# Kernel optimization log

Hardware: AMD Instinct MI355X
Metric: run time of the kernel (lower is better)

## Reference

```python
import jax, jax.numpy as jnp
import numpy as np

HIDDEN = 5120
HEAD_DIM = 128
HQ = 40
HKV = 8
NUM_MOD = 3
Q_SIZE = HQ * HEAD_DIM          # 5120
KV_SIZE = HKV * HEAD_DIM        # 1024
GATE = HQ                       # attn gating enabled
QKV_OUT = Q_SIZE + 2 * KV_SIZE + GATE  # 7208
EPS = 1e-6
N_TOK = 2048


def setup_inputs() -> dict:
    key = jax.random.key(0)
    ks = jax.random.split(key, 8)
    s = 0.02
    return {
        "hidden_states": jax.random.normal(ks[0], (N_TOK, HIDDEN), jnp.float32),
        "rope": jax.random.normal(ks[1], (N_TOK, HEAD_DIM), jnp.float32),
        "pre_norm_w": jax.random.normal(ks[2], (NUM_MOD * HIDDEN,), jnp.float32) * s,
        "qkv_w": jax.random.normal(ks[3], (NUM_MOD * QKV_OUT, HIDDEN), jnp.float32) * s,
        "q_norm_w": jax.random.normal(ks[4], (NUM_MOD * HEAD_DIM,), jnp.float32) * s,
        "k_norm_w": jax.random.normal(ks[5], (NUM_MOD * HEAD_DIM,), jnp.float32) * s,
        "proj_w": jax.random.normal(ks[6], (NUM_MOD * HIDDEN, Q_SIZE), jnp.float32) * s,
        "modality_ids": jax.random.randint(ks[7], (N_TOK,), 0, NUM_MOD, jnp.int64),
    }


def _mm_rmsnorm(x, w_flat, mids, dim):
    # per-token modality weight slice; residual parameterization (w + 1)
    w = w_flat.reshape(NUM_MOD, dim)[mids]  # [N, dim]
    if x.ndim == 3:
        w = w[:, None, :]  # broadcast over heads
    rms = jax.lax.rsqrt(jnp.mean(x * x, axis=-1, keepdims=True) + EPS)
    return x * rms * (w + 1.0)


def _moe_linear(x, w_flat, mids, out_f):
    # 3 GEMMs (one per expert), then per-token select -- same math as masked dispatch
    wm = w_flat.reshape(NUM_MOD, out_f, x.shape[-1])
    outs = jnp.einsum('nd,mod->nmo', x, wm)  # [N, 3, out_f]
    return jnp.take_along_axis(outs, mids[:, None, None], axis=1)[:, 0, :]


def _rotary(x, cos, sin):
    # x: [N, H, D]; cos/sin: [N, D/2]
    x1, x2 = jnp.split(x, 2, axis=-1)
    c = cos[:, None, :]
    s = sin[:, None, :]
    return jnp.concatenate([x1 * c - x2 * s, x1 * s + x2 * c], axis=-1)


def reference(hidden_states, rope, pre_norm_w, qkv_w, q_norm_w, k_norm_w, proj_w, modality_ids):
    N = hidden_states.shape[0]
    mids = modality_ids

    h = _mm_rmsnorm(hidden_states, pre_norm_w, mids, HIDDEN)
    qkv = _moe_linear(h, qkv_w, mids, QKV_OUT)  # [N, 7208]
    q, k, v, g = jnp.split(qkv, [Q_SIZE, Q_SIZE + KV_SIZE, Q_SIZE + 2 * KV_SIZE], axis=-1)
    q = q.reshape(N, HQ, HEAD_DIM)
    k = k.reshape(N, HKV, HEAD_DIM)
    v = v.reshape(N, HKV, HEAD_DIM)

    q = _mm_rmsnorm(q, q_norm_w, mids, HEAD_DIM)
    k = _mm_rmsnorm(k, k_norm_w, mids, HEAD_DIM)

    sin, cos = jnp.split(rope, 2, axis=-1)  # rope.chunk(2, dim=-1) -> sin, cos
    q = _rotary(q, cos, sin)
    k = _rotary(k, cos, sin)

    # GQA attention over the full token sequence
    G = HQ // HKV
    qg = q.reshape(N, HKV, G, HEAD_DIM)
    scale = 1.0 / np.sqrt(HEAD_DIM).astype(np.float32)
    scores = jnp.einsum('nkgd,mkd->kgnm', qg, k) * scale  # [8, 5, N, N]
    p = jax.nn.softmax(scores, axis=-1)
    o = jnp.einsum('kgnm,mkd->nkgd', p, v).reshape(N, HQ, HEAD_DIM)

    o = o * jax.nn.sigmoid(g)[:, :, None]  # attention gating per q-head
    o = o.reshape(N, Q_SIZE)
    return _moe_linear(o, proj_w, mids, HIDDEN)
```

## Files before the change

kernel.cpp:

```cpp
#include <hip/hip_runtime.h>
#include <hip/hip_bf16.h>

#define N_TOK 2048
#define HIDDEN 5120
#define HEAD_DIM 128
#define HQ 40
#define HKV 8
#define QKV_OUT 7208
#define Q_SIZE 5120
#define KV_SIZE 1024

typedef __attribute__((ext_vector_type(8))) short bf16x8;
typedef __attribute__((ext_vector_type(4))) float f32x4;
typedef __attribute__((ext_vector_type(4))) unsigned short us4;

__device__ inline unsigned short f2bf(float f) {
    return __builtin_bit_cast(unsigned short, __float2bfloat16(f));
}
__device__ inline float bf2f(unsigned short s) {
    unsigned u = ((unsigned)s) << 16;
    return __builtin_bit_cast(float, u);
}
__device__ inline f32x4 mfma16(bf16x8 a, bf16x8 b, f32x4 c) {
    return __builtin_amdgcn_mfma_f32_16x16x32_bf16(a, b, c, 0, 0, 0);
}
__device__ inline void gl16(const void* g, void* l) {
    __builtin_amdgcn_global_load_lds((__attribute__((address_space(1))) void*)g,
                                     (__attribute__((address_space(3))) void*)l, 16, 0, 0);
}

__global__ void k_sort(const int* __restrict__ mids_raw, int* __restrict__ meta,
                       int* __restrict__ perm) {
    int l = threadIdx.x;
    int oddnz = 0;
    for (int c = 0; c < 32; ++c) {
        int idx = c * 64 + l;
        int v = mids_raw[idx];
        if ((idx & 1) && v != 0) oddnz = 1;
    }
    bool is64 = (__ballot(oddnz) == 0ULL);
    int c0 = 0, c1 = 0;
    for (int c = 0; c < 32; ++c) {
        int i = c * 64 + l;
        int m = is64 ? mids_raw[2 * i] : mids_raw[i];
        c0 += (m == 0); c1 += (m == 1);
    }
    for (int o = 32; o; o >>= 1) { c0 += __shfl_xor(c0, o); c1 += __shfl_xor(c1, o); }
    if (l == 0) { meta[0] = 0; meta[1] = c0; meta[2] = c0 + c1; meta[3] = N_TOK; }
    int r0 = 0, r1 = c0, r2 = c0 + c1;
    unsigned long long below = (1ULL << l) - 1ULL;
    for (int c = 0; c < 32; ++c) {
        int i = c * 64 + l;
        int m = is64 ? mids_raw[2 * i] : mids_raw[i];
        unsigned long long b0 = __ballot(m == 0), b1 = __ballot(m == 1), b2 = __ballot(m == 2);
        int pos = (m == 0) ? r0 + __popcll(b0 & below)
                : (m == 1) ? r1 + __popcll(b1 & below)
                           : r2 + __popcll(b2 & below);
        perm[pos] = i;
        r0 += __popcll(b0); r1 += __popcll(b1); r2 += __popcll(b2);
    }
}

__global__ __launch_bounds__(256) void k_cvt(const float* __restrict__ src,
                                             unsigned short* __restrict__ dst, int n8) {
    int i = blockIdx.x * 256 + threadIdx.x;
    int stride = gridDim.x * 256;
    for (; i < n8; i += stride) {
        float4 a = ((const float4*)src)[2 * i];
        float4 b = ((const float4*)src)[2 * i + 1];
        bf16x8 o;
        o[0] = (short)f2bf(a.x); o[1] = (short)f2bf(a.y);
        o[2] = (short)f2bf(a.z); o[3] = (short)f2bf(a.w);
        o[4] = (short)f2bf(b.x); o[5] = (short)f2bf(b.y);
        o[6] = (short)f2bf(b.z); o[7] = (short)f2bf(b.w);
        ((bf16x8*)dst)[i] = o;
    }
}

__global__ __launch_bounds__(256) void k_prenorm(const float* __restrict__ hidden,
        const float* __restrict__ pnw, const int* __restrict__ meta,
        const int* __restrict__ perm, unsigned short* __restrict__ h) {
    int i = blockIdx.x;
    int m = (i >= meta[1]) + (i >= meta[2]);
    int t = perm[i];
    const float4* x = (const float4*)(hidden + (size_t)t * HIDDEN);
    const float4* wv = (const float4*)(pnw + (size_t)m * HIDDEN);
    int tid = threadIdx.x;
    float4 xv[5];
    float ss = 0.f;
#pragma unroll
    for (int j = 0; j < 5; ++j) {
        xv[j] = x[tid + j * 256];
        ss += xv[j].x * xv[j].x + xv[j].y * xv[j].y + xv[j].z * xv[j].z + xv[j].w * xv[j].w;
    }
    for (int o = 32; o; o >>= 1) ss += __shfl_xor(ss, o);
    __shared__ float red[4];
    if ((tid & 63) == 0) red[tid >> 6] = ss;
    __syncthreads();
    float rms = rsqrtf((red[0] + red[1] + red[2] + red[3]) * (1.f / HIDDEN) + 1e-6f);
    us4* dst = (us4*)(h + (size_t)i * HIDDEN);
#pragma unroll
    for (int j = 0; j < 5; ++j) {
        float4 w = wv[tid + j * 256];
        us4 o4;
        o4.x = f2bf(xv[j].x * rms * (w.x + 1.f));
        o4.y = f2bf(xv[j].y * rms * (w.y + 1.f));
        o4.z = f2bf(xv[j].z * rms * (w.z + 1.f));
        o4.w = f2bf(xv[j].w * rms * (w.w + 1.f));
        dst[tid + j * 256] = o4;
    }
}

template <int NOUT, bool SCATTER>
__global__ __launch_bounds__(256, 2) void k_gemm(
        const unsigned short* __restrict__ A, const unsigned short* __restrict__ Bw,
        unsigned short* __restrict__ outB, float* __restrict__ outF,
        const int* __restrict__ meta, const int* __restrict__ perm,
        int nx, int ny) {
    int nwg = nx * ny * 3;
    int bid = blockIdx.x;
    int xcd = bid & 7, o = bid >> 3;
    int q = nwg >> 3, r = nwg & 7;
    int swz = (xcd < r ? xcd * (q + 1) : r * (q + 1) + (xcd - r) * q) + o;
    int mz = swz / (nx * ny);
    int rest = swz - mz * (nx * ny);
    int ty = rest / nx, tx = rest - ty * nx;

    int rowS = meta[mz], rowE = meta[mz + 1];
    int row0 = rowS + tx * 128;
    if (row0 >= rowE) return;
    int col0 = ty * 128;
    const unsigned short* Bm = Bw + (size_t)mz * NOUT * HIDDEN;

    __shared__ __align__(16) char smem[65536];
    int tid = threadIdx.x, l = tid & 63, w = tid >> 6;
    int wr = (w >> 1) * 64, wc = (w & 1) * 64;

    f32x4 acc[4][4] = {};

    const int lr = l >> 3, lc = l & 7;
    const int sch = (lc ^ lr) * 8;
    const unsigned short* ag[4];
    const unsigned short* bg[4];
#pragma unroll
    for (int j = 0; j < 4; ++j) {
        int ar = row0 + 32 * j + 8 * w + lr;
        if (ar > rowE - 1) ar = rowE - 1;
        ag[j] = A + (size_t)ar * HIDDEN + sch;
        int bc = col0 + 32 * j + 8 * w + lr;
        if (bc > NOUT - 1) bc = NOUT - 1;
        bg[j] = Bm + (size_t)bc * HIDDEN + sch;
    }
    char* asw = smem + w * 1024;
    char* bsw = smem + 16384 + w * 1024;

    auto STAGE = [&](int buf, int kk) {
#pragma unroll
        for (int j = 0; j < 4; ++j) {
            gl16(ag[j] + kk, asw + buf * 32768 + j * 4096);
            gl16(bg[j] + kk, bsw + buf * 32768 + j * 4096);
        }
    };
    auto COMPUTE = [&](int buf) {
        char* baseA = smem + buf * 32768;
        char* baseB = baseA + 16384;
#pragma unroll
        for (int ks = 0; ks < 2; ++ks) {
            bf16x8 af[4], bfm[4];
#pragma unroll
            for (int mi = 0; mi < 4; ++mi) {
                int row = wr + mi * 16 + (l & 15);
                af[mi] = *(const bf16x8*)(baseA + row * 128 +
                            ((ks * 64 + (l >> 4) * 16) ^ ((row & 7) << 4)));
            }
#pragma unroll
            for (int ni = 0; ni < 4; ++ni) {
                int row = wc + ni * 16 + (l & 15);
                bfm[ni] = *(const bf16x8*)(baseB + row * 128 +
                            ((ks * 64 + (l >> 4) * 16) ^ ((row & 7) << 4)));
            }
#pragma unroll
            for (int mi = 0; mi < 4; ++mi)
#pragma unroll
                for (int ni = 0; ni < 4; ++ni)
                    acc[mi][ni] = mfma16(af[mi], bfm[ni], acc[mi][ni]);
        }
    };

    STAGE(0, 0);
    asm volatile("s_waitcnt vmcnt(0)" ::: "memory");
    __builtin_amdgcn_sched_barrier(0);
    __builtin_amdgcn_s_barrier();
    __builtin_amdgcn_sched_barrier(0);
    int cur = 0;
#pragma unroll 1
    for (int kt = 0; kt < HIDDEN / 64 - 1; ++kt) {
        STAGE(cur ^ 1, (kt + 1) * 64);
        COMPUTE(cur);
        asm volatile("s_waitcnt vmcnt(0) lgkmcnt(0)" ::: "memory");
        __builtin_amdgcn_sched_barrier(0);
        __builtin_amdgcn_s_barrier();
        __builtin_amdgcn_sched_barrier(0);
        cur ^= 1;
    }
    COMPUTE(cur);

#pragma unroll
    for (int mi = 0; mi < 4; ++mi) {
        int rbase = row0 + wr + mi * 16 + ((l >> 4) << 2);
#pragma unroll
        for (int ni = 0; ni < 4; ++ni) {
            int col = col0 + wc + ni * 16 + (l & 15);
            if (col >= NOUT) continue;
#pragma unroll
            for (int rr = 0; rr < 4; ++rr) {
                int row = rbase + rr;
                if (row >= rowE) continue;
                if (SCATTER) {
                    int t = perm[row];
                    outF[(size_t)t * HIDDEN + col] = acc[mi][ni][rr];
                } else {
                    outB[(size_t)row * NOUT + col] = f2bf(acc[mi][ni][rr]);
                }
            }
        }
    }
}

template <int NOUT, bool SCATTER>
__global__ __launch_bounds__(256) void k_moe_gemm(
        const unsigned short* __restrict__ A, const float* __restrict__ B,
        unsigned short* __restrict__ outB, float* __restrict__ outF,
        const int* __restrict__ meta, const int* __restrict__ perm) {
    int mz = blockIdx.z;
    int rowS = meta[mz], rowE = meta[mz + 1];
    int row0 = rowS + blockIdx.y * 128;
    if (row0 >= rowE) return;
    int col0 = blockIdx.x * 128;
    const float* Bm = B + (size_t)mz * NOUT * HIDDEN;

    __shared__ __align__(16) unsigned short As[128 * 64];
    __shared__ __align__(16) unsigned short Bs[128 * 64];
    int tid = threadIdx.x, l = tid & 63, w = tid >> 6;
    int wr = (w >> 1) * 64, wc = (w & 1) * 64;

    f32x4 acc[4][4] = {};
    int sr = tid >> 1, half = tid & 1;
    int arow = row0 + sr;
    if (arow > N_TOK - 1) arow = N_TOK - 1;
    const unsigned short* aptr = A + (size_t)arow * HIDDEN + half * 32;
    int bcol = col0 + sr;
    bool bok = (bcol < NOUT);
    const float* bptr = Bm + (size_t)(bok ? bcol : 0) * HIDDEN + half * 32;

    char* awp[4]; char* bwp[4];
#pragma unroll
    for (int q = 0; q < 4; ++q) {
        int boff = sr * 128 + ((((half * 4 + q) * 16)) ^ ((sr & 7) << 4));
        awp[q] = (char*)As + boff;
        bwp[q] = (char*)Bs + boff;
    }

#pragma unroll 1
    for (int kk = 0; kk < HIDDEN; kk += 64) {
        bf16x8 av[4];
#pragma unroll
        for (int q = 0; q < 4; ++q) av[q] = *(const bf16x8*)(aptr + kk + q * 8);
        bf16x8 bw[4];
#pragma unroll
        for (int q = 0; q < 4; ++q) {
            float4 u, v;
            if (bok) {
                u = ((const float4*)(bptr + kk))[2 * q];
                v = ((const float4*)(bptr + kk))[2 * q + 1];
            } else {
                u = make_float4(0.f, 0.f, 0.f, 0.f);
                v = u;
            }
            bf16x8 pk;
            pk[0] = (short)f2bf(u.x); pk[1] = (short)f2bf(u.y);
            pk[2] = (short)f2bf(u.z); pk[3] = (short)f2bf(u.w);
            pk[4] = (short)f2bf(v.x); pk[5] = (short)f2bf(v.y);
            pk[6] = (short)f2bf(v.z); pk[7] = (short)f2bf(v.w);
            bw[q] = pk;
        }
        __syncthreads();
#pragma unroll
        for (int q = 0; q < 4; ++q) {
            *(bf16x8*)awp[q] = av[q];
            *(bf16x8*)bwp[q] = bw[q];
        }
        __syncthreads();
#pragma unroll
        for (int ks = 0; ks < 2; ++ks) {
            bf16x8 af[4], bfm[4];
#pragma unroll
            for (int mi = 0; mi < 4; ++mi) {
                int row = wr + mi * 16 + (l & 15);
                af[mi] = *(const bf16x8*)((char*)As + row * 128 +
                            ((ks * 64 + (l >> 4) * 16) ^ ((row & 7) << 4)));
            }
#pragma unroll
            for (int ni = 0; ni < 4; ++ni) {
                int row = wc + ni * 16 + (l & 15);
                bfm[ni] = *(const bf16x8*)((char*)Bs + row * 128 +
                            ((ks * 64 + (l >> 4) * 16) ^ ((row & 7) << 4)));
            }
#pragma unroll
            for (int mi = 0; mi < 4; ++mi)
#pragma unroll
                for (int ni = 0; ni < 4; ++ni)
                    acc[mi][ni] = mfma16(af[mi], bfm[ni], acc[mi][ni]);
        }
    }
#pragma unroll
    for (int mi = 0; mi < 4; ++mi) {
        int rbase = row0 + wr + mi * 16 + ((l >> 4) << 2);
#pragma unroll
        for (int ni = 0; ni < 4; ++ni) {
            int col = col0 + wc + ni * 16 + (l & 15);
            if (col >= NOUT) continue;
#pragma unroll
            for (int rr = 0; rr < 4; ++rr) {
                int row = rbase + rr;
                if (row >= rowE) continue;
                if (SCATTER) {
                    int t = perm[row];
                    outF[(size_t)t * HIDDEN + col] = acc[mi][ni][rr];
                } else {
                    outB[(size_t)row * NOUT + col] = f2bf(acc[mi][ni][rr]);
                }
            }
        }
    }
}

__global__ __launch_bounds__(256) void k_qknorm(const unsigned short* __restrict__ qkv,
        const float* __restrict__ rope, const float* __restrict__ qnw,
        const float* __restrict__ knw, const int* __restrict__ meta,
        const int* __restrict__ perm, unsigned short* __restrict__ qb,
        unsigned short* __restrict__ kb, float* __restrict__ gate) {
    int i = blockIdx.x;
    int m = (i >= meta[1]) + (i >= meta[2]);
    int t = perm[i];
    int tid = threadIdx.x, w = tid >> 6, l = tid & 63;
    const unsigned short* base = qkv + (size_t)i * QKV_OUT;
    const float* rp = rope + (size_t)t * HEAD_DIM;
    const float qscale = 0.08838834764831845f * 1.4426950408889634f;
    for (int hh = w; hh < 48; hh += 4) {
        bool isq = hh < 40;
        const unsigned short* src = base + (isq ? hh * 128 : Q_SIZE + (hh - 40) * 128);
        float x0 = bf2f(src[2 * l]), x1 = bf2f(src[2 * l + 1]);
        float ss = x0 * x0 + x1 * x1;
        for (int o = 32; o; o >>= 1) ss += __shfl_xor(ss, o);
        float rms = rsqrtf(ss * (1.f / 128.f) + 1e-6f);
        const float* nw = (isq ? qnw : knw) + m * 128;
        float y0 = x0 * rms * (nw[2 * l] + 1.f);
        float y1 = x1 * rms * (nw[2 * l + 1] + 1.f);
        float p0 = __shfl_xor(y0, 32);
        float p1 = __shfl_xor(y1, 32);
        float r0v, r1v;
        if (l < 32) {
            int d = 2 * l;
            r0v = y0 * rp[64 + d] - p0 * rp[d];
            r1v = y1 * rp[64 + d + 1] - p1 * rp[d + 1];
        } else {
            int d = 2 * l - 64;
            r0v = p0 * rp[d] + y0 * rp[64 + d];
            r1v = p1 * rp[d + 1] + y1 * rp[64 + d + 1];
        }
        if (isq) {
            r0v *= qscale; r1v *= qscale;
            unsigned short* dst = qb + (size_t)i * Q_SIZE + hh * 128 + 2 * l;
            dst[0] = f2bf(r0v); dst[1] = f2bf(r1v);
        } else {
            unsigned short* dst = kb + (size_t)i * KV_SIZE + (hh - 40) * 128 + 2 * l;
            dst[0] = f2bf(r0v); dst[1] = f2bf(r1v);
        }
    }
    if (tid < HQ) {
        float g = bf2f(base[Q_SIZE + 2 * KV_SIZE + tid]);
        gate[(size_t)i * HQ + tid] = 1.f / (1.f + expf(-g));
    }
}

__global__ __launch_bounds__(256) void k_vtrans(const unsigned short* __restrict__ qkv,
                                                unsigned short* __restrict__ vT) {
    int t0 = blockIdx.x * 64, db = blockIdx.y * 64, kvh = blockIdx.z;
    __shared__ unsigned short tile[64][68];
    int tid = threadIdx.x;
    int tr = tid >> 2, seg = tid & 3;
    const unsigned short* src = qkv + (size_t)(t0 + tr) * QKV_OUT + Q_SIZE + KV_SIZE +
                                kvh * 128 + db + seg * 16;
    us4* drow = (us4*)&tile[tr][seg * 16];
#pragma unroll
    for (int q = 0; q < 4; ++q) drow[q] = ((const us4*)src)[q];
    __syncthreads();
    int dr = tid >> 2;
    unsigned short* dst = vT + ((size_t)kvh * 128 + db + dr) * N_TOK + t0 + seg * 16;
    unsigned short buf[16];
#pragma unroll
    for (int j = 0; j < 16; ++j) buf[j] = tile[seg * 16 + j][dr];
#pragma unroll
    for (int q = 0; q < 4; ++q) ((us4*)dst)[q] = ((us4*)buf)[q];
}

__global__ __launch_bounds__(256) void k_attn(
        const unsigned short* __restrict__ qb,
        const unsigned short* __restrict__ kb,
        const unsigned short* __restrict__ vT,
        const float* __restrict__ gate,
        unsigned short* __restrict__ og) {
    int qt = blockIdx.x, qh = blockIdx.y, kvh = qh / 5;
    int tid = threadIdx.x, w = tid >> 6, l = tid & 63;
    int q0 = qt * 128 + w * 32;
    __shared__ __align__(16) char smem[49152];
    char* Ks = smem;
    char* Vs = smem + 16384;
    char* Ps = smem + 32768 + w * 4096;

    bf16x8 qf[2][4];
#pragma unroll
    for (int mi = 0; mi < 2; ++mi)
#pragma unroll
        for (int ks = 0; ks < 4; ++ks)
            qf[mi][ks] = *(const bf16x8*)(qb + (size_t)(q0 + mi * 16 + (l & 15)) * Q_SIZE +
                                          qh * 128 + ks * 32 + (l >> 4) * 8);

    f32x4 oacc[2][8] = {};
    f32x4 psum[2] = {};

    int kr = tid >> 2, kseg = tid & 3;
    int vr = tid >> 1, vh2 = tid & 1;

#pragma unroll 1
    for (int kt = 0; kt < 32; ++kt) {
        int t0 = kt * 64;
        bf16x8 kv4[4], vv4[4];
        const unsigned short* ksrc = kb + (size_t)(t0 + kr) * KV_SIZE + kvh * 128 + kseg * 32;
        const unsigned short* vsrc = vT + ((size_t)kvh * 128 + vr) * N_TOK + t0 + vh2 * 32;
#pragma unroll
        for (int q = 0; q < 4; ++q) {
            kv4[q] = *(const bf16x8*)(ksrc + q * 8);
            vv4[q] = *(const bf16x8*)(vsrc + q * 8);
        }
        __syncthreads();
#pragma unroll
        for (int q = 0; q < 4; ++q) {
            *(bf16x8*)(Ks + kr * 256 + ((((kseg * 4 + q) * 16)) ^ ((kr & 7) << 4))) = kv4[q];
            *(bf16x8*)(Vs + vr * 128 + ((((vh2 * 4 + q) * 16)) ^ ((vr & 7) << 4))) = vv4[q];
        }
        __syncthreads();
        f32x4 s[2][4] = {};
#pragma unroll
        for (int ks = 0; ks < 4; ++ks) {
            bf16x8 kf[4];
#pragma unroll
            for (int ni = 0; ni < 4; ++ni) {
                int row = ni * 16 + (l & 15);
                kf[ni] = *(const bf16x8*)(Ks + row * 256 +
                            ((ks * 64 + (l >> 4) * 16) ^ ((row & 7) << 4)));
            }
#pragma unroll
            for (int mi = 0; mi < 2; ++mi)
#pragma unroll
                for (int ni = 0; ni < 4; ++ni)
                    s[mi][ni] = mfma16(qf[mi][ks], kf[ni], s[mi][ni]);
        }
#pragma unroll
        for (int mi = 0; mi < 2; ++mi)
#pragma unroll
            for (int ni = 0; ni < 4; ++ni) {
#pragma unroll
                for (int r = 0; r < 4; ++r) {
                    float p = exp2f(s[mi][ni][r]);
                    psum[mi][r] += p;
                    int qr = mi * 16 + ((l >> 4) << 2) + r;
                    int tcb = (ni * 16 + (l & 15)) * 2;
                    *(unsigned short*)(Ps + qr * 128 +
                        (tcb ^ (((qr >> 2) & 3) << 5))) = f2bf(p);
                }
            }
#pragma unroll
        for (int ks = 0; ks < 2; ++ks) {
            bf16x8 pa[2];
#pragma unroll
            for (int mi = 0; mi < 2; ++mi) {
                int qr = mi * 16 + (l & 15);
                pa[mi] = *(const bf16x8*)(Ps + qr * 128 +
                            ((ks * 64 + (l >> 4) * 16) ^ (((qr >> 2) & 3) << 5)));
            }
#pragma unroll
            for (int nd = 0; nd < 8; ++nd) {
                int row = nd * 16 + (l & 15);
                bf16x8 vf = *(const bf16x8*)(Vs + row * 128 +
                            ((ks * 64 + (l >> 4) * 16) ^ ((row & 7) << 4)));
#pragma unroll
                for (int mi = 0; mi < 2; ++mi)
                    oacc[mi][nd] = mfma16(pa[mi], vf, oacc[mi][nd]);
            }
        }
    }
#pragma unroll
    for (int mi = 0; mi < 2; ++mi)
#pragma unroll
        for (int r = 0; r < 4; ++r) {
            float v = psum[mi][r];
            v += __shfl_xor(v, 1);
            v += __shfl_xor(v, 2);
            v += __shfl_xor(v, 4);
            v += __shfl_xor(v, 8);
            psum[mi][r] = v;
        }
#pragma unroll
    for (int mi = 0; mi < 2; ++mi)
#pragma unroll
        for (int r = 0; r < 4; ++r) {
            int row = q0 + mi * 16 + ((l >> 4) << 2) + r;
            float sc = (1.f / psum[mi][r]) * gate[(size_t)row * HQ + qh];
#pragma unroll
            for (int nd = 0; nd < 8; ++nd)
                og[(size_t)row * Q_SIZE + qh * 128 + nd * 16 + (l & 15)] =
                    f2bf(oacc[mi][nd][r] * sc);
        }
}

extern "C" void kernel_launch(void* const* d_in, const int* in_sizes, int n_in,
                              void* d_out, int out_size, void* d_ws, size_t ws_size,
                              hipStream_t stream) {
    const float* hidden = (const float*)d_in[0];
    const float* rope   = (const float*)d_in[1];
    const float* pnw    = (const float*)d_in[2];
    const float* qkvw   = (const float*)d_in[3];
    const float* qnw    = (const float*)d_in[4];
    const float* knw    = (const float*)d_in[5];
    const float* projw  = (const float*)d_in[6];
    const int*   mids   = (const int*)d_in[7];
    float* out = (float*)d_out;

    char* ws = (char*)d_ws;
    const size_t nqkvw = (size_t)3 * QKV_OUT * HIDDEN;
    const size_t nprojw = (size_t)3 * HIDDEN * Q_SIZE;
    const size_t wbytes = (nqkvw + nprojw) * 2;

    const size_t small_bytes = 16384 +
        (size_t)N_TOK * HIDDEN * 2 +
        (size_t)N_TOK * QKV_OUT * 2 +
        (size_t)N_TOK * Q_SIZE * 2 +
        (size_t)N_TOK * KV_SIZE * 2 +
        (size_t)N_TOK * KV_SIZE * 2 +
        (size_t)N_TOK * Q_SIZE * 2 +
        (size_t)N_TOK * HQ * 4;
    bool use_bf = (ws_size >= wbytes + small_bytes);
    if (!use_bf && ws_size < small_bytes) return;

    unsigned short* wqkv = (unsigned short*)ws;
    unsigned short* wproj = wqkv + nqkvw;
    char* sb = ws + (use_bf ? wbytes : 0);

    int* meta = (int*)sb;
    int* perm = (int*)(sb + 64);
    unsigned short* h   = (unsigned short*)(sb + 16384);
    unsigned short* qkv = h   + (size_t)N_TOK * HIDDEN;
    unsigned short* qb  = qkv + (size_t)N_TOK * QKV_OUT;
    unsigned short* kb  = qb  + (size_t)N_TOK * Q_SIZE;
    unsigned short* vT  = kb  + (size_t)N_TOK * KV_SIZE;
    unsigned short* og  = vT  + (size_t)N_TOK * KV_SIZE;
    float* gate = (float*)(og + (size_t)N_TOK * Q_SIZE);

    k_sort<<<1, 64, 0, stream>>>(mids, meta, perm);
    if (use_bf) {
        k_cvt<<<2048, 256, 0, stream>>>(qkvw, wqkv, (int)(nqkvw / 8));
        k_cvt<<<2048, 256, 0, stream>>>(projw, wproj, (int)(nprojw / 8));
    }
    k_prenorm<<<2048, 256, 0, stream>>>(hidden, pnw, meta, perm, h);
    if (use_bf)
        k_gemm<QKV_OUT, false><<<16 * 57 * 3, 256, 0, stream>>>(
            h, wqkv, qkv, nullptr, meta, perm, 16, 57);
    else
        k_moe_gemm<QKV_OUT, false><<<dim3(57, 16, 3), 256, 0, stream>>>(
            h, qkvw, qkv, nullptr, meta, perm);
    k_qknorm<<<2048, 256, 0, stream>>>(qkv, rope, qnw, knw, meta, perm, qb, kb, gate);
    k_vtrans<<<dim3(32, 2, 8), 256, 0, stream>>>(qkv, vT);
    k_attn<<<dim3(16, 40), 256, 0, stream>>>(qb, kb, vT, gate, og);
    if (use_bf)
        k_gemm<HIDDEN, true><<<16 * 40 * 3, 256, 0, stream>>>(
            og, wproj, nullptr, out, meta, perm, 16, 40);
    else
        k_moe_gemm<HIDDEN, true><<<dim3(40, 16, 3), 256, 0, stream>>>(
            og, projw, nullptr, out, meta, perm);
}
```

Before: 958.6 us.

## Fuse fp32-to-bf16 weight conversion into the MoE GEMM B-tile load

```diff
diff --git a/kernel.cpp b/kernel.cpp
--- a/kernel.cpp
+++ b/kernel.cpp
@@ -61,22 +61,6 @@
     }
 }
 
-__global__ __launch_bounds__(256) void k_cvt(const float* __restrict__ src,
-                                             unsigned short* __restrict__ dst, int n8) {
-    int i = blockIdx.x * 256 + threadIdx.x;
-    int stride = gridDim.x * 256;
-    for (; i < n8; i += stride) {
-        float4 a = ((const float4*)src)[2 * i];
-        float4 b = ((const float4*)src)[2 * i + 1];
-        bf16x8 o;
-        o[0] = (short)f2bf(a.x); o[1] = (short)f2bf(a.y);
-        o[2] = (short)f2bf(a.z); o[3] = (short)f2bf(a.w);
-        o[4] = (short)f2bf(b.x); o[5] = (short)f2bf(b.y);
-        o[6] = (short)f2bf(b.z); o[7] = (short)f2bf(b.w);
-        ((bf16x8*)dst)[i] = o;
-    }
-}
-
 __global__ __launch_bounds__(256) void k_prenorm(const float* __restrict__ hidden,
         const float* __restrict__ pnw, const int* __restrict__ meta,
         const int* __restrict__ perm, unsigned short* __restrict__ h) {
@@ -113,7 +97,7 @@
 
 template <int NOUT, bool SCATTER>
 __global__ __launch_bounds__(256, 2) void k_gemm(
-        const unsigned short* __restrict__ A, const unsigned short* __restrict__ Bw,
+        const unsigned short* __restrict__ A, const float* __restrict__ Bw,
         unsigned short* __restrict__ outB, float* __restrict__ outF,
         const int* __restrict__ meta, const int* __restrict__ perm,
         int nx, int ny) {
@@ -130,7 +114,7 @@
     int row0 = rowS + tx * 128;
     if (row0 >= rowE) return;
     int col0 = ty * 128;
-    const unsigned short* Bm = Bw + (size_t)mz * NOUT * HIDDEN;
+    const float* Bm = Bw + (size_t)mz * NOUT * HIDDEN;
 
     __shared__ __align__(16) char smem[65536];
     int tid = threadIdx.x, l = tid & 63, w = tid >> 6;
@@ -141,24 +125,44 @@
     const int lr = l >> 3, lc = l & 7;
     const int sch = (lc ^ lr) * 8;
     const unsigned short* ag[4];
-    const unsigned short* bg[4];
 #pragma unroll
     for (int j = 0; j < 4; ++j) {
         int ar = row0 + 32 * j + 8 * w + lr;
         if (ar > rowE - 1) ar = rowE - 1;
         ag[j] = A + (size_t)ar * HIDDEN + sch;
+    }
+    const float* bg[4];
+    int brow[4];
+#pragma unroll
+    for (int j = 0; j < 4; ++j) {
         int bc = col0 + 32 * j + 8 * w + lr;
         if (bc > NOUT - 1) bc = NOUT - 1;
-        bg[j] = Bm + (size_t)bc * HIDDEN + sch;
+        bg[j] = Bm + (size_t)bc * HIDDEN + lc * 8;
+        brow[j] = 32 * j + 8 * w + lr;
     }
     char* asw = smem + w * 1024;
-    char* bsw = smem + 16384 + w * 1024;
-
+
+    float4 breg[4][2];
     auto STAGE = [&](int buf, int kk) {
 #pragma unroll
+        for (int j = 0; j < 4; ++j) gl16(ag[j] + kk, asw + buf * 32768 + j * 4096);
+#pragma unroll
         for (int j = 0; j < 4; ++j) {
-            gl16(ag[j] + kk, asw + buf * 32768 + j * 4096);
-            gl16(bg[j] + kk, bsw + buf * 32768 + j * 4096);
+            breg[j][0] = *(const float4*)(bg[j] + kk);
+            breg[j][1] = *(const float4*)(bg[j] + kk + 4);
+        }
+    };
+    auto BWRITE = [&](int buf) {
+#pragma unroll
+        for (int j = 0; j < 4; ++j) {
+            bf16x8 pk;
+            pk[0] = (short)f2bf(breg[j][0].x); pk[1] = (short)f2bf(breg[j][0].y);
+            pk[2] = (short)f2bf(breg[j][0].z); pk[3] = (short)f2bf(breg[j][0].w);
+            pk[4] = (short)f2bf(breg[j][1].x); pk[5] = (short)f2bf(breg[j][1].y);
+            pk[6] = (short)f2bf(breg[j][1].z); pk[7] = (short)f2bf(breg[j][1].w);
+            int row = brow[j];
+            *(bf16x8*)(smem + buf * 32768 + 16384 + row * 128 +
+                       ((lc * 16) ^ ((row & 7) << 4))) = pk;
         }
     };
     auto COMPUTE = [&](int buf) {
@@ -188,7 +192,8 @@
     };
 
     STAGE(0, 0);
-    asm volatile("s_waitcnt vmcnt(0)" ::: "memory");
+    BWRITE(0);
+    asm volatile("s_waitcnt vmcnt(0) lgkmcnt(0)" ::: "memory");
     __builtin_amdgcn_sched_barrier(0);
     __builtin_amdgcn_s_barrier();
     __builtin_amdgcn_sched_barrier(0);
@@ -197,6 +202,7 @@
     for (int kt = 0; kt < HIDDEN / 64 - 1; ++kt) {
         STAGE(cur ^ 1, (kt + 1) * 64);
         COMPUTE(cur);
+        BWRITE(cur ^ 1);
         asm volatile("s_waitcnt vmcnt(0) lgkmcnt(0)" ::: "memory");
         __builtin_amdgcn_sched_barrier(0);
         __builtin_amdgcn_s_barrier();
@@ -205,114 +211,6 @@
     }
     COMPUTE(cur);
 
-#pragma unroll
-    for (int mi = 0; mi < 4; ++mi) {
-        int rbase = row0 + wr + mi * 16 + ((l >> 4) << 2);
-#pragma unroll
-        for (int ni = 0; ni < 4; ++ni) {
-            int col = col0 + wc + ni * 16 + (l & 15);
-            if (col >= NOUT) continue;
-#pragma unroll
-            for (int rr = 0; rr < 4; ++rr) {
-                int row = rbase + rr;
-                if (row >= rowE) continue;
-                if (SCATTER) {
-                    int t = perm[row];
-                    outF[(size_t)t * HIDDEN + col] = acc[mi][ni][rr];
-                } else {
-                    outB[(size_t)row * NOUT + col] = f2bf(acc[mi][ni][rr]);
-                }
-            }
-        }
-    }
-}
-
-template <int NOUT, bool SCATTER>
-__global__ __launch_bounds__(256) void k_moe_gemm(
-        const unsigned short* __restrict__ A, const float* __restrict__ B,
-        unsigned short* __restrict__ outB, float* __restrict__ outF,
-        const int* __restrict__ meta, const int* __restrict__ perm) {
-    int mz = blockIdx.z;
-    int rowS = meta[mz], rowE = meta[mz + 1];
-    int row0 = rowS + blockIdx.y * 128;
-    if (row0 >= rowE) return;
-    int col0 = blockIdx.x * 128;
-    const float* Bm = B + (size_t)mz * NOUT * HIDDEN;
-
-    __shared__ __align__(16) unsigned short As[128 * 64];
-    __shared__ __align__(16) unsigned short Bs[128 * 64];
-    int tid = threadIdx.x, l = tid & 63, w = tid >> 6;
-    int wr = (w >> 1) * 64, wc = (w & 1) * 64;
-
-    f32x4 acc[4][4] = {};
-    int sr = tid >> 1, half = tid & 1;
-    int arow = row0 + sr;
-    if (arow > N_TOK - 1) arow = N_TOK - 1;
-    const unsigned short* aptr = A + (size_t)arow * HIDDEN + half * 32;
-    int bcol = col0 + sr;
-    bool bok = (bcol < NOUT);
-    const float* bptr = Bm + (size_t)(bok ? bcol : 0) * HIDDEN + half * 32;
-
-    char* awp[4]; char* bwp[4];
-#pragma unroll
-    for (int q = 0; q < 4; ++q) {
-        int boff = sr * 128 + ((((half * 4 + q) * 16)) ^ ((sr & 7) << 4));
-        awp[q] = (char*)As + boff;
-        bwp[q] = (char*)Bs + boff;
-    }
-
-#pragma unroll 1
-    for (int kk = 0; kk < HIDDEN; kk += 64) {
-        bf16x8 av[4];
-#pragma unroll
-        for (int q = 0; q < 4; ++q) av[q] = *(const bf16x8*)(aptr + kk + q * 8);
-        bf16x8 bw[4];
-#pragma unroll
-        for (int q = 0; q < 4; ++q) {
-            float4 u, v;
-            if (bok) {
-                u = ((const float4*)(bptr + kk))[2 * q];
-                v = ((const float4*)(bptr + kk))[2 * q + 1];
-            } else {
-                u = make_float4(0.f, 0.f, 0.f, 0.f);
-                v = u;
-            }
-            bf16x8 pk;
-            pk[0] = (short)f2bf(u.x); pk[1] = (short)f2bf(u.y);
-            pk[2] = (short)f2bf(u.z); pk[3] = (short)f2bf(u.w);
-            pk[4] = (short)f2bf(v.x); pk[5] = (short)f2bf(v.y);
-            pk[6] = (short)f2bf(v.z); pk[7] = (short)f2bf(v.w);
-            bw[q] = pk;
-        }
-        __syncthreads();
-#pragma unroll
-        for (int q = 0; q < 4; ++q) {
-            *(bf16x8*)awp[q] = av[q];
-            *(bf16x8*)bwp[q] = bw[q];
-        }
-        __syncthreads();
-#pragma unroll
-        for (int ks = 0; ks < 2; ++ks) {
-            bf16x8 af[4], bfm[4];
-#pragma unroll
-            for (int mi = 0; mi < 4; ++mi) {
-                int row = wr + mi * 16 + (l & 15);
-                af[mi] = *(const bf16x8*)((char*)As + row * 128 +
-                            ((ks * 64 + (l >> 4) * 16) ^ ((row & 7) << 4)));
-            }
-#pragma unroll
-            for (int ni = 0; ni < 4; ++ni) {
-                int row = wc + ni * 16 + (l & 15);
-                bfm[ni] = *(const bf16x8*)((char*)Bs + row * 128 +
-                            ((ks * 64 + (l >> 4) * 16) ^ ((row & 7) << 4)));
-            }
-#pragma unroll
-            for (int mi = 0; mi < 4; ++mi)
-#pragma unroll
-                for (int ni = 0; ni < 4; ++ni)
-                    acc[mi][ni] = mfma16(af[mi], bfm[ni], acc[mi][ni]);
-        }
-    }
 #pragma unroll
     for (int mi = 0; mi < 4; ++mi) {
         int rbase = row0 + wr + mi * 16 + ((l >> 4) << 2);
@@ -539,10 +437,6 @@
     float* out = (float*)d_out;
 
     char* ws = (char*)d_ws;
-    const size_t nqkvw = (size_t)3 * QKV_OUT * HIDDEN;
-    const size_t nprojw = (size_t)3 * HIDDEN * Q_SIZE;
-    const size_t wbytes = (nqkvw + nprojw) * 2;
-
     const size_t small_bytes = 16384 +
         (size_t)N_TOK * HIDDEN * 2 +
         (size_t)N_TOK * QKV_OUT * 2 +
@@ -551,16 +445,11 @@
         (size_t)N_TOK * KV_SIZE * 2 +
         (size_t)N_TOK * Q_SIZE * 2 +
         (size_t)N_TOK * HQ * 4;
-    bool use_bf = (ws_size >= wbytes + small_bytes);
-    if (!use_bf && ws_size < small_bytes) return;
-
-    unsigned short* wqkv = (unsigned short*)ws;
-    unsigned short* wproj = wqkv + nqkvw;
-    char* sb = ws + (use_bf ? wbytes : 0);
-
-    int* meta = (int*)sb;
-    int* perm = (int*)(sb + 64);
-    unsigned short* h   = (unsigned short*)(sb + 16384);
+    if (ws_size < small_bytes) return;
+
+    int* meta = (int*)ws;
+    int* perm = (int*)(ws + 64);
+    unsigned short* h   = (unsigned short*)(ws + 16384);
     unsigned short* qkv = h   + (size_t)N_TOK * HIDDEN;
     unsigned short* qb  = qkv + (size_t)N_TOK * QKV_OUT;
     unsigned short* kb  = qb  + (size_t)N_TOK * Q_SIZE;
@@ -569,24 +458,12 @@
     float* gate = (float*)(og + (size_t)N_TOK * Q_SIZE);
 
     k_sort<<<1, 64, 0, stream>>>(mids, meta, perm);
-    if (use_bf) {
-        k_cvt<<<2048, 256, 0, stream>>>(qkvw, wqkv, (int)(nqkvw / 8));
-        k_cvt<<<2048, 256, 0, stream>>>(projw, wproj, (int)(nprojw / 8));
-    }
     k_prenorm<<<2048, 256, 0, stream>>>(hidden, pnw, meta, perm, h);
-    if (use_bf)
-        k_gemm<QKV_OUT, false><<<16 * 57 * 3, 256, 0, stream>>>(
-            h, wqkv, qkv, nullptr, meta, perm, 16, 57);
-    else
-        k_moe_gemm<QKV_OUT, false><<<dim3(57, 16, 3), 256, 0, stream>>>(
-            h, qkvw, qkv, nullptr, meta, perm);
+    k_gemm<QKV_OUT, false><<<16 * 57 * 3, 256, 0, stream>>>(
+        h, qkvw, qkv, nullptr, meta, perm, 16, 57);
     k_qknorm<<<2048, 256, 0, stream>>>(qkv, rope, qnw, knw, meta, perm, qb, kb, gate);
     k_vtrans<<<dim3(32, 2, 8), 256, 0, stream>>>(qkv, vT);
     k_attn<<<dim3(16, 40), 256, 0, stream>>>(qb, kb, vT, gate, og);
-    if (use_bf)
-        k_gemm<HIDDEN, true><<<16 * 40 * 3, 256, 0, stream>>>(
-            og, wproj, nullptr, out, meta, perm, 16, 40);
-    else
-        k_moe_gemm<HIDDEN, true><<<dim3(40, 16, 3), 256, 0, stream>>>(
-            og, projw, nullptr, out, meta, perm);
-}
+    k_gemm<HIDDEN, true><<<16 * 40 * 3, 256, 0, stream>>>(
+        og, projw, nullptr, out, meta, perm, 16, 40);
+}
```

New measurement: 927.2 us. -3.3%, faster.

## Deepen GEMM pipeline to 4-stage ring with BK=32 and partial vmcnt waits

Applied to the files above, without the earlier changes.

```diff
diff --git a/kernel.cpp b/kernel.cpp
--- a/kernel.cpp
+++ b/kernel.cpp
@@ -138,72 +138,73 @@
 
     f32x4 acc[4][4] = {};
 
-    const int lr = l >> 3, lc = l & 7;
-    const int sch = (lc ^ lr) * 8;
-    const unsigned short* ag[4];
-    const unsigned short* bg[4];
-#pragma unroll
-    for (int j = 0; j < 4; ++j) {
-        int ar = row0 + 32 * j + 8 * w + lr;
+    const int lr = l >> 2, lc = l & 3;
+    const int sch = (lc ^ (lr & 3)) * 8;
+    const unsigned short* ag[2];
+    const unsigned short* bg[2];
+#pragma unroll
+    for (int j = 0; j < 2; ++j) {
+        int ar = row0 + 64 * j + 16 * w + lr;
         if (ar > rowE - 1) ar = rowE - 1;
         ag[j] = A + (size_t)ar * HIDDEN + sch;
-        int bc = col0 + 32 * j + 8 * w + lr;
+        int bc = col0 + 64 * j + 16 * w + lr;
         if (bc > NOUT - 1) bc = NOUT - 1;
         bg[j] = Bm + (size_t)bc * HIDDEN + sch;
     }
-    char* asw = smem + w * 1024;
-    char* bsw = smem + 16384 + w * 1024;
-
-    auto STAGE = [&](int buf, int kk) {
-#pragma unroll
-        for (int j = 0; j < 4; ++j) {
-            gl16(ag[j] + kk, asw + buf * 32768 + j * 4096);
-            gl16(bg[j] + kk, bsw + buf * 32768 + j * 4096);
-        }
+
+    auto STAGE = [&](int buf, int ktile) {
+        int kk = ktile * 32;
+        char* base = smem + buf * 16384 + w * 1024;
+#pragma unroll
+        for (int j = 0; j < 2; ++j) gl16(ag[j] + kk, base + j * 4096);
+#pragma unroll
+        for (int j = 0; j < 2; ++j) gl16(bg[j] + kk, base + 8192 + j * 4096);
+        __builtin_amdgcn_sched_barrier(0);
     };
     auto COMPUTE = [&](int buf) {
-        char* baseA = smem + buf * 32768;
-        char* baseB = baseA + 16384;
-#pragma unroll
-        for (int ks = 0; ks < 2; ++ks) {
-            bf16x8 af[4], bfm[4];
-#pragma unroll
-            for (int mi = 0; mi < 4; ++mi) {
-                int row = wr + mi * 16 + (l & 15);
-                af[mi] = *(const bf16x8*)(baseA + row * 128 +
-                            ((ks * 64 + (l >> 4) * 16) ^ ((row & 7) << 4)));
-            }
-#pragma unroll
-            for (int ni = 0; ni < 4; ++ni) {
-                int row = wc + ni * 16 + (l & 15);
-                bfm[ni] = *(const bf16x8*)(baseB + row * 128 +
-                            ((ks * 64 + (l >> 4) * 16) ^ ((row & 7) << 4)));
-            }
-#pragma unroll
-            for (int mi = 0; mi < 4; ++mi)
-#pragma unroll
-                for (int ni = 0; ni < 4; ++ni)
-                    acc[mi][ni] = mfma16(af[mi], bfm[ni], acc[mi][ni]);
-        }
+        char* baseA = smem + buf * 16384;
+        char* baseB = baseA + 8192;
+        bf16x8 af[4], bfm[4];
+#pragma unroll
+        for (int mi = 0; mi < 4; ++mi) {
+            int row = wr + mi * 16 + (l & 15);
+            af[mi] = *(const bf16x8*)(baseA + row * 64 +
+                        (((l >> 4) << 4) ^ ((row & 3) << 4)));
+        }
+#pragma unroll
+        for (int ni = 0; ni < 4; ++ni) {
+            int row = wc + ni * 16 + (l & 15);
+            bfm[ni] = *(const bf16x8*)(baseB + row * 64 +
+                        (((l >> 4) << 4) ^ ((row & 3) << 4)));
+        }
+#pragma unroll
+        for (int mi = 0; mi < 4; ++mi)
+#pragma unroll
+            for (int ni = 0; ni < 4; ++ni)
+                acc[mi][ni] = mfma16(af[mi], bfm[ni], acc[mi][ni]);
     };
 
-    STAGE(0, 0);
-    asm volatile("s_waitcnt vmcnt(0)" ::: "memory");
+    const int NKT = HIDDEN / 32;
+    STAGE(0, 0); STAGE(1, 1); STAGE(2, 2);
+#pragma unroll 1
+    for (int kt = 0; kt < NKT - 2; ++kt) {
+        asm volatile("s_waitcnt vmcnt(8) lgkmcnt(0)" ::: "memory");
+        __builtin_amdgcn_sched_barrier(0);
+        __builtin_amdgcn_s_barrier();
+        __builtin_amdgcn_sched_barrier(0);
+        if (kt + 3 < NKT) STAGE((kt + 3) & 3, kt + 3);
+        COMPUTE(kt & 3);
+    }
+    asm volatile("s_waitcnt vmcnt(4) lgkmcnt(0)" ::: "memory");
     __builtin_amdgcn_sched_barrier(0);
     __builtin_amdgcn_s_barrier();
     __builtin_amdgcn_sched_barrier(0);
-    int cur = 0;
-#pragma unroll 1
-    for (int kt = 0; kt < HIDDEN / 64 - 1; ++kt) {
-        STAGE(cur ^ 1, (kt + 1) * 64);
-        COMPUTE(cur);
-        asm volatile("s_waitcnt vmcnt(0) lgkmcnt(0)" ::: "memory");
-        __builtin_amdgcn_sched_barrier(0);
-        __builtin_amdgcn_s_barrier();
-        __builtin_amdgcn_sched_barrier(0);
-        cur ^= 1;
-    }
-    COMPUTE(cur);
+    COMPUTE((NKT - 2) & 3);
+    asm volatile("s_waitcnt vmcnt(0) lgkmcnt(0)" ::: "memory");
+    __builtin_amdgcn_sched_barrier(0);
+    __builtin_amdgcn_s_barrier();
+    __builtin_amdgcn_sched_barrier(0);
+    COMPUTE((NKT - 1) & 3);
 
 #pragma unroll
     for (int mi = 0; mi < 4; ++mi) {
```

Result: no change. 976.9 us (+1.9%).

## Overlap weight conversion with prenorm and attention; wider-tile proj GEMM

Applied to the files above, without the earlier changes.

```diff
diff --git a/kernel.cpp b/kernel.cpp
--- a/kernel.cpp
+++ b/kernel.cpp
@@ -27,6 +27,20 @@
 __device__ inline void gl16(const void* g, void* l) {
     __builtin_amdgcn_global_load_lds((__attribute__((address_space(1))) void*)g,
                                      (__attribute__((address_space(3))) void*)l, 16, 0, 0);
+}
+__device__ inline void cvt_chunk(const float* __restrict__ src,
+                                 unsigned short* __restrict__ dst,
+                                 int n8, int i, int stride) {
+    for (; i < n8; i += stride) {
+        float4 a = ((const float4*)src)[2 * i];
+        float4 b = ((const float4*)src)[2 * i + 1];
+        bf16x8 o;
+        o[0] = (short)f2bf(a.x); o[1] = (short)f2bf(a.y);
+        o[2] = (short)f2bf(a.z); o[3] = (short)f2bf(a.w);
+        o[4] = (short)f2bf(b.x); o[5] = (short)f2bf(b.y);
+        o[6] = (short)f2bf(b.z); o[7] = (short)f2bf(b.w);
+        ((bf16x8*)dst)[i] = o;
+    }
 }
 
 __global__ void k_sort(const int* __restrict__ mids_raw, int* __restrict__ meta,
@@ -61,31 +75,23 @@
     }
 }
 
-__global__ __launch_bounds__(256) void k_cvt(const float* __restrict__ src,
-                                             unsigned short* __restrict__ dst, int n8) {
-    int i = blockIdx.x * 256 + threadIdx.x;
-    int stride = gridDim.x * 256;
-    for (; i < n8; i += stride) {
-        float4 a = ((const float4*)src)[2 * i];
-        float4 b = ((const float4*)src)[2 * i + 1];
-        bf16x8 o;
-        o[0] = (short)f2bf(a.x); o[1] = (short)f2bf(a.y);
-        o[2] = (short)f2bf(a.z); o[3] = (short)f2bf(a.w);
-        o[4] = (short)f2bf(b.x); o[5] = (short)f2bf(b.y);
-        o[6] = (short)f2bf(b.z); o[7] = (short)f2bf(b.w);
-        ((bf16x8*)dst)[i] = o;
-    }
-}
-
-__global__ __launch_bounds__(256) void k_prenorm(const float* __restrict__ hidden,
+__global__ __launch_bounds__(256) void k_prenorm_cvt(const float* __restrict__ hidden,
         const float* __restrict__ pnw, const int* __restrict__ meta,
-        const int* __restrict__ perm, unsigned short* __restrict__ h) {
-    int i = blockIdx.x;
+        const int* __restrict__ perm, unsigned short* __restrict__ h,
+        const float* __restrict__ csrc, unsigned short* __restrict__ cdst, int n8) {
+    int bid = blockIdx.x;
+    int tid = threadIdx.x;
+    if (bid >= 2048) {
+        int b = bid - 2048;
+        int stride = (gridDim.x - 2048) * 256;
+        cvt_chunk(csrc, cdst, n8, b * 256 + tid, stride);
+        return;
+    }
+    int i = bid;
     int m = (i >= meta[1]) + (i >= meta[2]);
     int t = perm[i];
     const float4* x = (const float4*)(hidden + (size_t)t * HIDDEN);
     const float4* wv = (const float4*)(pnw + (size_t)m * HIDDEN);
-    int tid = threadIdx.x;
     float4 xv[5];
     float ss = 0.f;
 #pragma unroll
@@ -210,6 +216,105 @@
         int rbase = row0 + wr + mi * 16 + ((l >> 4) << 2);
 #pragma unroll
         for (int ni = 0; ni < 4; ++ni) {
+            int col = col0 + wc + ni * 16 + (l & 15);
+            if (col >= NOUT) continue;
+#pragma unroll
+            for (int rr = 0; rr < 4; ++rr) {
+                int row = rbase + rr;
+                if (row >= rowE) continue;
+                if (SCATTER) {
+                    int t = perm[row];
+                    outF[(size_t)t * HIDDEN + col] = acc[mi][ni][rr];
+                } else {
+                    outB[(size_t)row * NOUT + col] = f2bf(acc[mi][ni][rr]);
+                }
+            }
+        }
+    }
+}
+
+template <int NOUT, bool SCATTER>
+__global__ __launch_bounds__(256, 2) void k_gemm2(
+        const unsigned short* __restrict__ A, const unsigned short* __restrict__ Bw,
+        unsigned short* __restrict__ outB, float* __restrict__ outF,
+        const int* __restrict__ meta, const int* __restrict__ perm,
+        int nx, int ny) {
+    int nwg = nx * ny * 3;
+    int bid = blockIdx.x;
+    int xcd = bid & 7, o = bid >> 3;
+    int q = nwg >> 3, r = nwg & 7;
+    int swz = (xcd < r ? xcd * (q + 1) : r * (q + 1) + (xcd - r) * q) + o;
+    int mz = swz / (nx * ny);
+    int rest = swz - mz * (nx * ny);
+    int ty = rest / nx, tx = rest - ty * nx;
+
+    int rowS = meta[mz], rowE = meta[mz + 1];
+    int row0 = rowS + tx * 128;
+    if (row0 >= rowE) return;
+    int col0 = ty * 256;
+    const unsigned short* Bm = Bw + (size_t)mz * NOUT * HIDDEN;
+
+    __shared__ __align__(16) unsigned short As[128 * 64];
+    __shared__ __align__(16) unsigned short Bs[256 * 64];
+    int tid = threadIdx.x, l = tid & 63, w = tid >> 6;
+    int wr = (w >> 1) * 64, wc = (w & 1) * 128;
+
+    f32x4 acc[4][8] = {};
+
+    const int lr = l >> 3, lc = l & 7;
+    const int sch = (lc ^ lr) * 8;
+    const unsigned short* ag[4];
+    const unsigned short* bg[8];
+#pragma unroll
+    for (int j = 0; j < 4; ++j) {
+        int ar = row0 + 32 * j + 8 * w + lr;
+        if (ar > rowE - 1) ar = rowE - 1;
+        ag[j] = A + (size_t)ar * HIDDEN + sch;
+    }
+#pragma unroll
+    for (int j = 0; j < 8; ++j) {
+        int bc = col0 + 32 * j + 8 * w + lr;
+        if (bc > NOUT - 1) bc = NOUT - 1;
+        bg[j] = Bm + (size_t)bc * HIDDEN + sch;
+    }
+    char* asw = (char*)As + w * 1024;
+    char* bsw = (char*)Bs + w * 1024;
+
+#pragma unroll 1
+    for (int kk = 0; kk < HIDDEN; kk += 64) {
+#pragma unroll
+        for (int j = 0; j < 4; ++j) gl16(ag[j] + kk, asw + j * 4096);
+#pragma unroll
+        for (int j = 0; j < 8; ++j) gl16(bg[j] + kk, bsw + j * 4096);
+        __syncthreads();
+#pragma unroll
+        for (int ks = 0; ks < 2; ++ks) {
+            bf16x8 af[4], bfm[8];
+#pragma unroll
+            for (int mi = 0; mi < 4; ++mi) {
+                int row = wr + mi * 16 + (l & 15);
+                af[mi] = *(const bf16x8*)((char*)As + row * 128 +
+                            ((ks * 64 + (l >> 4) * 16) ^ ((row & 7) << 4)));
+            }
+#pragma unroll
+            for (int ni = 0; ni < 8; ++ni) {
+                int row = wc + ni * 16 + (l & 15);
+                bfm[ni] = *(const bf16x8*)((char*)Bs + row * 128 +
+                            ((ks * 64 + (l >> 4) * 16) ^ ((row & 7) << 4)));
+            }
+#pragma unroll
+            for (int mi = 0; mi < 4; ++mi)
+#pragma unroll
+                for (int ni = 0; ni < 8; ++ni)
+                    acc[mi][ni] = mfma16(af[mi], bfm[ni], acc[mi][ni]);
+        }
+        __syncthreads();
+    }
+#pragma unroll
+    for (int mi = 0; mi < 4; ++mi) {
+        int rbase = row0 + wr + mi * 16 + ((l >> 4) << 2);
+#pragma unroll
+        for (int ni = 0; ni < 8; ++ni) {
             int col = col0 + wc + ni * 16 + (l & 15);
             if (col >= NOUT) continue;
 #pragma unroll
@@ -405,14 +510,23 @@
     for (int q = 0; q < 4; ++q) ((us4*)dst)[q] = ((us4*)buf)[q];
 }
 
-__global__ __launch_bounds__(256) void k_attn(
+__global__ __launch_bounds__(256) void k_attn_cvt(
         const unsigned short* __restrict__ qb,
         const unsigned short* __restrict__ kb,
         const unsigned short* __restrict__ vT,
         const float* __restrict__ gate,
-        unsigned short* __restrict__ og) {
-    int qt = blockIdx.x, qh = blockIdx.y, kvh = qh / 5;
-    int tid = threadIdx.x, w = tid >> 6, l = tid & 63;
+        unsigned short* __restrict__ og,
+        const float* __restrict__ csrc, unsigned short* __restrict__ cdst, int n8) {
+    int bid = blockIdx.x;
+    int tid = threadIdx.x;
+    if (bid >= 640) {
+        int b = bid - 640;
+        int stride = (gridDim.x - 640) * 256;
+        cvt_chunk(csrc, cdst, n8, b * 256 + tid, stride);
+        return;
+    }
+    int qt = bid & 15, qh = bid >> 4, kvh = qh / 5;
+    int w = tid >> 6, l = tid & 63;
     int q0 = qt * 128 + w * 32;
     __shared__ __align__(16) char smem[49152];
     char* Ks = smem;
@@ -570,23 +684,26 @@
 
     k_sort<<<1, 64, 0, stream>>>(mids, meta, perm);
     if (use_bf) {
-        k_cvt<<<2048, 256, 0, stream>>>(qkvw, wqkv, (int)(nqkvw / 8));
-        k_cvt<<<2048, 256, 0, stream>>>(projw, wproj, (int)(nprojw / 8));
-    }
-    k_prenorm<<<2048, 256, 0, stream>>>(hidden, pnw, meta, perm, h);
-    if (use_bf)
+        k_prenorm_cvt<<<2048 + 1024, 256, 0, stream>>>(
+            hidden, pnw, meta, perm, h, qkvw, wqkv, (int)(nqkvw / 8));
         k_gemm<QKV_OUT, false><<<16 * 57 * 3, 256, 0, stream>>>(
             h, wqkv, qkv, nullptr, meta, perm, 16, 57);
-    else
+        k_qknorm<<<2048, 256, 0, stream>>>(qkv, rope, qnw, knw, meta, perm, qb, kb, gate);
+        k_vtrans<<<dim3(32, 2, 8), 256, 0, stream>>>(qkv, vT);
+        k_attn_cvt<<<640 + 1024, 256, 0, stream>>>(
+            qb, kb, vT, gate, og, projw, wproj, (int)(nprojw / 8));
+        k_gemm2<HIDDEN, true><<<16 * 20 * 3, 256, 0, stream>>>(
+            og, wproj, nullptr, out, meta, perm, 16, 20);
+    } else {
+        k_prenorm_cvt<<<2048, 256, 0, stream>>>(
+            hidden, pnw, meta, perm, h, nullptr, nullptr, 0);
         k_moe_gemm<QKV_OUT, false><<<dim3(57, 16, 3), 256, 0, stream>>>(
             h, qkvw, qkv, nullptr, meta, perm);
-    k_qknorm<<<2048, 256, 0, stream>>>(qkv, rope, qnw, knw, meta, perm, qb, kb, gate);
-    k_vtrans<<<dim3(32, 2, 8), 256, 0, stream>>>(qkv, vT);
-    k_attn<<<dim3(16, 40), 256, 0, stream>>>(qb, kb, vT, gate, og);
-    if (use_bf)
-        k_gemm<HIDDEN, true><<<16 * 40 * 3, 256, 0, stream>>>(
-            og, wproj, nullptr, out, meta, perm, 16, 40);
-    else
+        k_qknorm<<<2048, 256, 0, stream>>>(qkv, rope, qnw, knw, meta, perm, qb, kb, gate);
+        k_vtrans<<<dim3(32, 2, 8), 256, 0, stream>>>(qkv, vT);
+        k_attn_cvt<<<640, 256, 0, stream>>>(
+            qb, kb, vT, gate, og, nullptr, nullptr, 0);
         k_moe_gemm<HIDDEN, true><<<dim3(40, 16, 3), 256, 0, stream>>>(
             og, projw, nullptr, out, meta, perm);
-}
+    }
+}
```

Result: faster. 919.1 us (-4.1%).
